# Optimization experiments

Hardware: AMD Instinct MI355X
Metric: run time of the kernel (lower is better)

## Reference

```python
import jax, jax.numpy as jnp
import numpy as np

N_MSB = 4
WB = 8       # weight bits
ABNM = 8     # activation bits for non-MVM ops
NL = 0.1     # noise level
B, IN, H = 256, 1024, 1024


def pact_a(x, a):
    # sign(x) * 0.5 * (|x| - ||x|-a| + a)  == sign(x)*min(|x|, a) for a>0
    return jnp.sign(x) * 0.5 * (jnp.abs(x) - jnp.abs(jnp.abs(x) - a) + a)


def _quant_val(x, bits, x_range):
    step = 2.0 ** (bits - 1)
    x01 = jnp.clip(x / x_range, -1.0 + 1.0 / step, 1.0 - 1.0 / step)
    return jnp.round(x01 * step) / step * x_range


def quant_ste(x, bits, x_range):
    # QuantFunc: straight-through estimator (identity grad wrt x, none wrt range)
    return x + jax.lax.stop_gradient(_quant_val(x, bits, x_range) - x)


def bitsplit(x, n_msb):
    # x in [0,1] -> n_msb binary planes stacked on axis 0, plus beta coefficients
    l1 = 2.0 ** n_msb - 1.0
    ys, betas = [], []
    for i in range(n_msb):
        l2 = 2.0 ** (n_msb - (i + 1))
        betas.append(l2 / l1)
        ys.append(jnp.mod(jnp.floor(jnp.round(l1 * x) / l2), 2.0))
    return jnp.stack(ys), jnp.asarray(betas, dtype=x.dtype)


def noisy_qmm(x, w, b, eps_w, eps_b):
    # CustomMM_bmm: quantized weights + gaussian noise in fwd; STE-style bwd.
    w_eff = w + jax.lax.stop_gradient(_quant_val(w, WB, 1.0) - w + eps_w * jnp.max(w) * NL)
    b_eff = b + jax.lax.stop_gradient(_quant_val(b, WB, 1.0) - b + eps_b * jnp.max(b) * NL)
    return jnp.einsum('nbi,nio->nbo', x, w_eff) + b_eff  # [n_msb, B, 4H]


def lstm_cell_q_bs(input, hx, cx, weight_ih, weight_hh, bias_ih, bias_hh,
                   eps_w_ih, eps_w_hh, eps_b_ih, eps_b_hh,
                   a1, a3, a4, a5, a6, a7, a8, a9, a10, a11):
    inp01 = (pact_a(input, a1) + a1) / (a1 * 2.0)            # [B, IN] in [0,1]
    inp_msb, beta = bitsplit(inp01, N_MSB)                   # [n_msb,B,IN], [n_msb]
    o1 = noisy_qmm(inp_msb, weight_ih, bias_ih, eps_w_ih, eps_b_ih)
    o2 = noisy_qmm(inp_msb, weight_hh, bias_hh, eps_w_hh, eps_b_hh)
    out = (o1 > 0.5).astype(inp01.dtype) + (o2 > 0.5).astype(inp01.dtype)
    gates = jnp.einsum('n,nbo->bo', beta, out)               # part1; part2 undefined in source -> 0
    i, j, f, o = jnp.split(gates, 4, axis=1)                 # each [B, H]
    forget_gate_out = quant_ste(pact_a(jax.nn.sigmoid(f), a3), ABNM, a3)
    input_gate_out = quant_ste(pact_a(jax.nn.sigmoid(i), a4), ABNM, a4)
    activation_out = quant_ste(pact_a(jnp.tanh(j), a5), ABNM, a5)
    output_gate_out = quant_ste(pact_a(jax.nn.sigmoid(o), a6), ABNM, a6)
    gated_cell = quant_ste(pact_a(cx * forget_gate_out, a7), ABNM, a7)
    activated_input = quant_ste(pact_a(input_gate_out * activation_out, a8), ABNM, a8)
    new_c = quant_ste(pact_a(gated_cell + activated_input, a9), ABNM, a9)
    activated_cell = quant_ste(pact_a(jnp.tanh(new_c), a10), ABNM, a10)
    new_h = quant_ste(pact_a(activated_cell * output_gate_out, a11), ABNM, a11)
    return new_h, new_c


def setup_inputs() -> dict:
    key = jax.random.key(0)
    ks = jax.random.split(key, 12)
    d = {
        'input': jax.random.normal(ks[0], (B, IN), jnp.float32),
        'hx': jax.random.normal(ks[1], (B, H), jnp.float32),
        'cx': jax.random.normal(ks[2], (B, H), jnp.float32),
        'weight_ih': jax.random.normal(ks[3], (N_MSB, IN, 4 * H), jnp.float32),
        'weight_hh': jax.random.normal(ks[4], (N_MSB, IN, 4 * H), jnp.float32),
        'bias_ih': jax.random.normal(ks[5], (N_MSB, 1, 4 * H), jnp.float32),
        'bias_hh': jax.random.normal(ks[6], (N_MSB, 1, 4 * H), jnp.float32),
        'eps_w_ih': jax.random.normal(ks[7], (N_MSB, IN, 4 * H), jnp.float32),
        'eps_w_hh': jax.random.normal(ks[8], (N_MSB, IN, 4 * H), jnp.float32),
        'eps_b_ih': jax.random.normal(ks[9], (N_MSB, 1, 4 * H), jnp.float32),
        'eps_b_hh': jax.random.normal(ks[10], (N_MSB, 1, 4 * H), jnp.float32),
    }
    a_init = {'a1': 128.0, 'a3': 1.0, 'a4': 1.0, 'a5': 1.0, 'a6': 1.0,
              'a7': 4.0, 'a8': 1.0, 'a9': 4.0, 'a10': 1.0, 'a11': 4.0}
    for name, v in a_init.items():
        d[name] = jnp.array([v], jnp.float32)
    return d


def reference(input, hx, cx, weight_ih, weight_hh, bias_ih, bias_hh,
              eps_w_ih, eps_w_hh, eps_b_ih, eps_b_hh,
              a1, a3, a4, a5, a6, a7, a8, a9, a10, a11):
    return lstm_cell_q_bs(input, hx, cx, weight_ih, weight_hh, bias_ih, bias_hh,
                          eps_w_ih, eps_w_hh, eps_b_ih, eps_b_hh,
                          a1, a3, a4, a5, a6, a7, a8, a9, a10, a11)
```

## Files before the change

### kernel.cpp

```cpp
#include <hip/hip_runtime.h>
#include <hip/hip_bf16.h>
#include <math.h>

typedef int   v4i __attribute__((ext_vector_type(4)));
typedef float v4f __attribute__((ext_vector_type(4)));

#define B_DIM   256
#define IN_DIM  1024
#define H4      4096
#define NPLANE  4
#define WELEM   (NPLANE * IN_DIM * H4)
#define XELEM   (B_DIM * IN_DIM)

#define WS_THRESH_OFF 64
#define WS_X_OFF      (64 + 262144)
#define WS_CMP_OFF    (64 + 262144 + 1048576)

#define SYNC_LDS() __asm__ volatile("s_waitcnt lgkmcnt(0)\n\ts_barrier" ::: "memory")

__global__ void k_max(const float* __restrict__ wih, const float* __restrict__ whh,
                      const float* __restrict__ bih, const float* __restrict__ bhh,
                      float* __restrict__ outm) {
  int b = blockIdx.x, t = threadIdx.x;
  const v4f* p; int slot; size_t base; int iters;
  if (b < 2048)      { p = (const v4f*)wih; slot = 0; base = (size_t)b * 2048;          iters = 8;  }
  else if (b < 4096) { p = (const v4f*)whh; slot = 1; base = (size_t)(b - 2048) * 2048; iters = 8;  }
  else if (b == 4096){ p = (const v4f*)bih; slot = 2; base = 0;                          iters = 16; }
  else               { p = (const v4f*)bhh; slot = 3; base = 0;                          iters = 16; }
  float m = -3.4e38f;
#pragma unroll 4
  for (int it = 0; it < iters; ++it) {
    v4f v = p[base + (size_t)it * 256 + t];
    m = fmaxf(m, fmaxf(fmaxf(v.x, v.y), fmaxf(v.z, v.w)));
  }
#pragma unroll
  for (int off = 32; off >= 1; off >>= 1) m = fmaxf(m, __shfl_down(m, off, 64));
  __shared__ float sm[4];
  int w = t >> 6, ln = t & 63;
  if (ln == 0) sm[w] = m;
  __syncthreads();
  if (t == 0) {
    m = fmaxf(fmaxf(sm[0], sm[1]), fmaxf(sm[2], sm[3]));
    atomicMax((int*)&outm[slot], __float_as_int(m));
  }
}

__global__ void k_prep(const float* __restrict__ input,
                       const float* __restrict__ bih, const float* __restrict__ bhh,
                       const float* __restrict__ ebih, const float* __restrict__ ebhh,
                       const float* __restrict__ a1p, const float* __restrict__ maxm,
                       double* __restrict__ thresh, signed char* __restrict__ X) {
  int gid = blockIdx.x * 256 + threadIdx.x;
  if (blockIdx.x < 1024) {
    float a1 = a1p[0];
    float x = input[gid];
    float t = fabsf(x), u = fabsf(t - a1);
    float sg = (x > 0.f) ? 0.5f : ((x < 0.f) ? -0.5f : 0.f);
    float p = sg * ((t - u) + a1);
    float inp01 = (p + a1) / (a1 * 2.0f);
    float q = rintf(15.0f * inp01);
    int qi = (int)q;
#pragma unroll
    for (int pl = 0; pl < 4; ++pl)
      X[pl * XELEM + gid] = (signed char)((qi >> (3 - pl)) & 1);
  } else {
    int i2 = gid - 262144;
    int s = i2 >> 14; int r = i2 & 16383;
    const float* bp = s ? bhh : bih;
    const float* ep = s ? ebhh : ebih;
    float mb = maxm[2 + s];
    float bv = bp[r], ev = ep[r];
    float xc = fminf(fmaxf(bv, -0.9921875f), 0.9921875f);
    float qv = rintf(xc * 128.f) * 0.0078125f;
    float noise = (ev * mb) * 0.1f;
    float beff = bv + ((qv - bv) + noise);
    thresh[i2] = 0.5 - (double)beff;
  }
}

__global__ __launch_bounds__(512, 4) void k_gemm(
    const float* __restrict__ Wih, const float* __restrict__ Whh,
    const float* __restrict__ Eih, const float* __restrict__ Ehh,
    const float* __restrict__ maxm, const double* __restrict__ thresh,
    const signed char* __restrict__ X, unsigned char* __restrict__ cmp) {
  const int ntile = blockIdx.x;
  const int sp = blockIdx.y;
  const int s = sp >> 2, plane = sp & 3;
  const float* W = s ? Whh : Wih;
  const float* E = s ? Ehh : Eih;
  const float maxw = maxm[s];

  const int tid = threadIdx.x;
  const int wave = tid >> 6, lane = tid & 63, quad = lane >> 4, l15 = lane & 15;

  __shared__ __align__(16) signed char Blds[2][4][32][80];

  v4i acc[4][2][2];
#pragma unroll
  for (int d = 0; d < 4; ++d)
#pragma unroll
    for (int m = 0; m < 2; ++m)
#pragma unroll
      for (int n = 0; n < 2; ++n) acc[d][m][n] = (v4i){0, 0, 0, 0};

  const int sn  = tid & 31;
  const int skq = tid >> 5;
  const float* Wt = W + (size_t)plane * (IN_DIM * H4) + (size_t)(skq * 4) * H4 + ntile * 32 + sn;
  const float* Et = E + (size_t)plane * (IN_DIM * H4) + (size_t)(skq * 4) * H4 + ntile * 32 + sn;

  const signed char* Xp = X + plane * XELEM;
  const int arow0 = wave * 32 + l15;

  auto cw = [&](const float wv[4], const float ev[4], int bf) {
    int pk[4] = {0, 0, 0, 0};
#pragma unroll
    for (int j = 0; j < 4; ++j) {
      float w = wv[j], evv = ev[j];
      float xc = fminf(fmaxf(w, -0.9921875f), 0.9921875f);
      float qv = rintf(xc * 128.f) * 0.0078125f;
      float noise = (evv * maxw) * 0.1f;
      float a = w + ((qv - w) + noise);
      float x0 = a * 8.f;    float f0 = rintf(x0); float r0 = x0 - f0;
      float x1 = r0 * 128.f; float f1 = rintf(x1); float r1 = x1 - f1;
      float x2 = r1 * 128.f; float f2 = rintf(x2); float r2 = x2 - f2;
      float x3 = r2 * 128.f; float f3 = rintf(x3);
      pk[0] |= ((int)f0 & 0xff) << (8 * j);
      pk[1] |= ((int)f1 & 0xff) << (8 * j);
      pk[2] |= ((int)f2 & 0xff) << (8 * j);
      pk[3] |= ((int)f3 & 0xff) << (8 * j);
    }
#pragma unroll
    for (int d = 0; d < 4; ++d)
      *(int*)&Blds[bf][d][sn][skq * 4] = pk[d];
  };

  auto loadWE = [&](int ck, float wv[4], float ev[4]) {
    size_t o = (size_t)(ck * 64) * H4;
#pragma unroll
    for (int j = 0; j < 4; ++j) { wv[j] = Wt[o + (size_t)j * H4]; ev[j] = Et[o + (size_t)j * H4]; }
  };

  float wA[4], eA[4], wB[4], eB[4];
  loadWE(0, wA, eA);
  loadWE(1, wB, eB);
  cw(wA, eA, 0);
  v4i afr[2], anx[2];
  afr[0] = *(const v4i*)(Xp + (arow0)      * IN_DIM + quad * 16);
  afr[1] = *(const v4i*)(Xp + (arow0 + 16) * IN_DIM + quad * 16);
  anx[0] = *(const v4i*)(Xp + (arow0)      * IN_DIM + 64 + quad * 16);
  anx[1] = *(const v4i*)(Xp + (arow0 + 16) * IN_DIM + 64 + quad * 16);
  SYNC_LDS();

#pragma unroll
  for (int ch = 0; ch < 16; ++ch) {
    const int buf = ch & 1;
    float wN[4], eN[4];
    v4i aN[2];
    if (ch < 14) {
      loadWE(ch + 2, wN, eN);
      aN[0] = *(const v4i*)(Xp + (arow0)      * IN_DIM + (ch + 2) * 64 + quad * 16);
      aN[1] = *(const v4i*)(Xp + (arow0 + 16) * IN_DIM + (ch + 2) * 64 + quad * 16);
    }
#pragma unroll
    for (int d = 0; d < 4; ++d) {
#pragma unroll
      for (int ns = 0; ns < 2; ++ns) {
        v4i bfr = *(const v4i*)&Blds[buf][d][ns * 16 + l15][quad * 16];
        acc[d][0][ns] = __builtin_amdgcn_mfma_i32_16x16x64_i8(afr[0], bfr, acc[d][0][ns], 0, 0, 0);
        acc[d][1][ns] = __builtin_amdgcn_mfma_i32_16x16x64_i8(afr[1], bfr, acc[d][1][ns], 0, 0, 0);
      }
    }
    if (ch < 15) cw(wB, eB, buf ^ 1);
#pragma unroll
    for (int j = 0; j < 4; ++j) { wB[j] = wN[j]; eB[j] = eN[j]; }
    afr[0] = anx[0]; afr[1] = anx[1];
    anx[0] = aN[0];  anx[1] = aN[1];
    SYNC_LDS();
  }

  const double inv = 1.0 / 16777216.0;
  const double* thp = thresh + (size_t)sp * H4;
  unsigned char* cp = cmp + (size_t)sp * B_DIM * H4;
#pragma unroll
  for (int ms = 0; ms < 2; ++ms) {
#pragma unroll
    for (int ns = 0; ns < 2; ++ns) {
      int col = ntile * 32 + ns * 16 + l15;
      double th = thp[col];
#pragma unroll
      for (int r = 0; r < 4; ++r) {
        long long T = ((long long)acc[0][ms][ns][r] << 21) + ((long long)acc[1][ms][ns][r] << 14)
                    + ((long long)acc[2][ms][ns][r] << 7)  +  (long long)acc[3][ms][ns][r];
        int row = wave * 32 + ms * 16 + quad * 4 + r;
        cp[(size_t)row * H4 + col] = ((double)T * inv > th) ? 1 : 0;
      }
    }
  }
}

__device__ __forceinline__ float pact_(float x, float a) {
  float t = fabsf(x), u = fabsf(t - a);
  float sg = (x > 0.f) ? 0.5f : ((x < 0.f) ? -0.5f : 0.f);
  return sg * ((t - u) + a);
}
__device__ __forceinline__ float quant_(float x, float a) {
  float xr = x / a;
  xr = fminf(fmaxf(xr, -0.9921875f), 0.9921875f);
  return rintf(xr * 128.f) * 0.0078125f * a;
}
__device__ __forceinline__ float sigm_(float x) { return 1.0f / (1.0f + expf(-x)); }

__global__ void k_pointwise(const unsigned char* __restrict__ cmp, const float* __restrict__ cx,
                            const float* a3, const float* a4, const float* a5, const float* a6,
                            const float* a7, const float* a8, const float* a9, const float* a10,
                            const float* a11, float* __restrict__ out) {
  int idx = blockIdx.x * 256 + threadIdx.x;
  int b = idx >> 10, h = idx & 1023;
  float g[4];
#pragma unroll
  for (int gi = 0; gi < 4; ++gi) {
    int col = gi * 1024 + h;
    float acc = 0.f;
#pragma unroll
    for (int n = 0; n < 4; ++n) {
      int o = (int)cmp[((size_t)(0 * 4 + n) * B_DIM + b) * H4 + col]
            + (int)cmp[((size_t)(1 * 4 + n) * B_DIM + b) * H4 + col];
      float beta = (float)(8 >> n) / 15.0f;
      acc = acc + beta * (float)o;
    }
    g[gi] = acc;
  }
  float fg = quant_(pact_(sigm_(g[2]), a3[0]), a3[0]);
  float ig = quant_(pact_(sigm_(g[0]), a4[0]), a4[0]);
  float ac = quant_(pact_(tanhf(g[1]), a5[0]), a5[0]);
  float og = quant_(pact_(sigm_(g[3]), a6[0]), a6[0]);
  float cxv = cx[idx];
  float gc = quant_(pact_(cxv * fg, a7[0]), a7[0]);
  float ai = quant_(pact_(ig * ac, a8[0]), a8[0]);
  float nc = quant_(pact_(gc + ai, a9[0]), a9[0]);
  float acl = quant_(pact_(tanhf(nc), a10[0]), a10[0]);
  float nh = quant_(pact_(acl * og, a11[0]), a11[0]);
  out[idx] = nh;
  out[XELEM + idx] = nc;
}

extern "C" void kernel_launch(void* const* d_in, const int* in_sizes, int n_in,
                              void* d_out, int out_size, void* d_ws, size_t ws_size,
                              hipStream_t stream) {
  (void)in_sizes; (void)n_in; (void)out_size; (void)ws_size;
  const float* input = (const float*)d_in[0];
  const float* cx    = (const float*)d_in[2];
  const float* wih   = (const float*)d_in[3];
  const float* whh   = (const float*)d_in[4];
  const float* bih   = (const float*)d_in[5];
  const float* bhh   = (const float*)d_in[6];
  const float* ewih  = (const float*)d_in[7];
  const float* ewhh  = (const float*)d_in[8];
  const float* ebih  = (const float*)d_in[9];
  const float* ebhh  = (const float*)d_in[10];
  const float* a1    = (const float*)d_in[11];
  const float* a3    = (const float*)d_in[12];
  const float* a4    = (const float*)d_in[13];
  const float* a5    = (const float*)d_in[14];
  const float* a6    = (const float*)d_in[15];
  const float* a7    = (const float*)d_in[16];
  const float* a8    = (const float*)d_in[17];
  const float* a9    = (const float*)d_in[18];
  const float* a10   = (const float*)d_in[19];
  const float* a11   = (const float*)d_in[20];
  float* out = (float*)d_out;

  char* ws = (char*)d_ws;
  float*         maxm   = (float*)ws;
  double*        thresh = (double*)(ws + WS_THRESH_OFF);
  signed char*   X      = (signed char*)(ws + WS_X_OFF);
  unsigned char* cmp    = (unsigned char*)(ws + WS_CMP_OFF);

  hipMemsetAsync(ws, 0, 64, stream);
  k_max<<<4098, 256, 0, stream>>>(wih, whh, bih, bhh, maxm);
  k_prep<<<1152, 256, 0, stream>>>(input, bih, bhh, ebih, ebhh, a1, maxm, thresh, X);
  k_gemm<<<dim3(128, 8), 512, 0, stream>>>(wih, whh, ewih, ewhh, maxm, thresh, X, cmp);
  k_pointwise<<<1024, 256, 0, stream>>>(cmp, cx, a3, a4, a5, a6, a7, a8, a9, a10, a11, out);
}
```

Measured before the change: 346.3 us.

## Stream W/E tiles into LDS via async global_load_lds triple buffer; two-pass max

The GEMM kernel now loads weight and noise tiles straight into a three-deep LDS ring with global_load_lds. Waits are explicit vmcnt counts, and each chunk is digitized from LDS into a double-buffered int8 tile before the MFMAs run. This removes register staging and is meant to overlap HBM streaming of the fp32 weights with compute. The max reduction changes from 4098 blocks with atomicMax plus a memset to 1026 blocks writing partial maxima, followed by a single-block reduce kernel. This adds LDS pressure (48KB raw) and an extra kernel launch, and the hand-written vmcnt counts must be exactly right.

Measured after the change: 347.0 us. Within noise of the previous version (+0.2%).

```diff
diff --git a/kernel.cpp b/kernel.cpp
--- a/kernel.cpp
+++ b/kernel.cpp
@@ -8,25 +8,25 @@
 #define B_DIM   256
 #define IN_DIM  1024
 #define H4      4096
-#define NPLANE  4
-#define WELEM   (NPLANE * IN_DIM * H4)
 #define XELEM   (B_DIM * IN_DIM)
 
 #define WS_THRESH_OFF 64
 #define WS_X_OFF      (64 + 262144)
 #define WS_CMP_OFF    (64 + 262144 + 1048576)
 
-#define SYNC_LDS() __asm__ volatile("s_waitcnt lgkmcnt(0)\n\ts_barrier" ::: "memory")
+#define BAR()   __asm__ volatile("s_barrier" ::: "memory")
+#define BARL()  __asm__ volatile("s_waitcnt lgkmcnt(0)\n\ts_barrier" ::: "memory")
+#define WVM(n)  __asm__ volatile("s_waitcnt vmcnt(" #n ")" ::: "memory")
 
 __global__ void k_max(const float* __restrict__ wih, const float* __restrict__ whh,
                       const float* __restrict__ bih, const float* __restrict__ bhh,
-                      float* __restrict__ outm) {
+                      float* __restrict__ part) {
   int b = blockIdx.x, t = threadIdx.x;
-  const v4f* p; int slot; size_t base; int iters;
-  if (b < 2048)      { p = (const v4f*)wih; slot = 0; base = (size_t)b * 2048;          iters = 8;  }
-  else if (b < 4096) { p = (const v4f*)whh; slot = 1; base = (size_t)(b - 2048) * 2048; iters = 8;  }
-  else if (b == 4096){ p = (const v4f*)bih; slot = 2; base = 0;                          iters = 16; }
-  else               { p = (const v4f*)bhh; slot = 3; base = 0;                          iters = 16; }
+  const v4f* p; size_t base; int iters;
+  if (b < 512)       { p = (const v4f*)wih; base = (size_t)b * 8192;         iters = 32; }
+  else if (b < 1024) { p = (const v4f*)whh; base = (size_t)(b - 512) * 8192; iters = 32; }
+  else if (b == 1024){ p = (const v4f*)bih; base = 0;                         iters = 16; }
+  else               { p = (const v4f*)bhh; base = 0;                         iters = 16; }
   float m = -3.4e38f;
 #pragma unroll 4
   for (int it = 0; it < iters; ++it) {
@@ -39,10 +39,24 @@
   int w = t >> 6, ln = t & 63;
   if (ln == 0) sm[w] = m;
   __syncthreads();
-  if (t == 0) {
-    m = fmaxf(fmaxf(sm[0], sm[1]), fmaxf(sm[2], sm[3]));
-    atomicMax((int*)&outm[slot], __float_as_int(m));
-  }
+  if (t == 0) part[b] = fmaxf(fmaxf(sm[0], sm[1]), fmaxf(sm[2], sm[3]));
+}
+
+__global__ void k_max2(const float* __restrict__ part, float* __restrict__ maxm) {
+  int t = threadIdx.x;
+  __shared__ float sm[4];
+#pragma unroll
+  for (int slot = 0; slot < 2; ++slot) {
+    float m = fmaxf(part[slot * 512 + t], part[slot * 512 + 256 + t]);
+#pragma unroll
+    for (int off = 32; off >= 1; off >>= 1) m = fmaxf(m, __shfl_down(m, off, 64));
+    int w = t >> 6, ln = t & 63;
+    if (ln == 0) sm[w] = m;
+    __syncthreads();
+    if (t == 0) maxm[slot] = fmaxf(fmaxf(sm[0], sm[1]), fmaxf(sm[2], sm[3]));
+    __syncthreads();
+  }
+  if (t == 0) { maxm[2] = part[1024]; maxm[3] = part[1025]; }
 }
 
 __global__ void k_prep(const float* __restrict__ input,
@@ -93,7 +107,8 @@
   const int tid = threadIdx.x;
   const int wave = tid >> 6, lane = tid & 63, quad = lane >> 4, l15 = lane & 15;
 
-  __shared__ __align__(16) signed char Blds[2][4][32][80];
+  __shared__ __align__(16) float raw[3][4096];
+  __shared__ __align__(16) signed char dbuf[2][4][32][80];
 
   v4i acc[4][2][2];
 #pragma unroll
@@ -103,22 +118,36 @@
 #pragma unroll
       for (int n = 0; n < 2; ++n) acc[d][m][n] = (v4i){0, 0, 0, 0};
 
-  const int sn  = tid & 31;
-  const int skq = tid >> 5;
-  const float* Wt = W + (size_t)plane * (IN_DIM * H4) + (size_t)(skq * 4) * H4 + ntile * 32 + sn;
-  const float* Et = E + (size_t)plane * (IN_DIM * H4) + (size_t)(skq * 4) * H4 + ntile * 32 + sn;
+  const int dr = wave * 8 + (lane >> 3);
+  const int dc = (lane & 7) * 4;
+  const size_t tbase = (size_t)plane * (IN_DIM * H4) + (size_t)ntile * 32;
+  const float* gW = W + tbase + (size_t)dr * H4 + dc;
+  const float* gE = E + tbase + (size_t)dr * H4 + dc;
 
   const signed char* Xp = X + plane * XELEM;
   const int arow0 = wave * 32 + l15;
 
-  auto cw = [&](const float wv[4], const float ev[4], int bf) {
+  auto dma = [&](int ch) {
+    const int rb = ch % 3;
+    const float* gw = gW + (size_t)(ch * 64) * H4;
+    const float* ge = gE + (size_t)(ch * 64) * H4;
+    __builtin_amdgcn_global_load_lds((const unsigned int*)gw,
+                                     (unsigned int*)&raw[rb][wave * 256], 16, 0, 0);
+    __builtin_amdgcn_global_load_lds((const unsigned int*)ge,
+                                     (unsigned int*)&raw[rb][2048 + wave * 256], 16, 0, 0);
+  };
+
+  const int sn = tid & 31, skq = tid >> 5;
+  auto digitize = [&](int ch) {
+    const int rb = ch % 3, db = ch & 1;
     int pk[4] = {0, 0, 0, 0};
 #pragma unroll
     for (int j = 0; j < 4; ++j) {
-      float w = wv[j], evv = ev[j];
+      float w  = raw[rb][(skq * 4 + j) * 32 + sn];
+      float ev = raw[rb][2048 + (skq * 4 + j) * 32 + sn];
       float xc = fminf(fmaxf(w, -0.9921875f), 0.9921875f);
       float qv = rintf(xc * 128.f) * 0.0078125f;
-      float noise = (evv * maxw) * 0.1f;
+      float noise = (ev * maxw) * 0.1f;
       float a = w + ((qv - w) + noise);
       float x0 = a * 8.f;    float f0 = rintf(x0); float r0 = x0 - f0;
       float x1 = r0 * 128.f; float f1 = rintf(x1); float r1 = x1 - f1;
@@ -131,51 +160,43 @@
     }
 #pragma unroll
     for (int d = 0; d < 4; ++d)
-      *(int*)&Blds[bf][d][sn][skq * 4] = pk[d];
+      *(int*)&dbuf[db][d][sn][skq * 4] = pk[d];
   };
 
-  auto loadWE = [&](int ck, float wv[4], float ev[4]) {
-    size_t o = (size_t)(ck * 64) * H4;
-#pragma unroll
-    for (int j = 0; j < 4; ++j) { wv[j] = Wt[o + (size_t)j * H4]; ev[j] = Et[o + (size_t)j * H4]; }
+  auto loadA = [&](int ch, v4i a[2]) {
+    a[0] = *(const v4i*)(Xp + (size_t)(arow0)      * IN_DIM + ch * 64 + quad * 16);
+    a[1] = *(const v4i*)(Xp + (size_t)(arow0 + 16) * IN_DIM + ch * 64 + quad * 16);
   };
 
-  float wA[4], eA[4], wB[4], eB[4];
-  loadWE(0, wA, eA);
-  loadWE(1, wB, eB);
-  cw(wA, eA, 0);
-  v4i afr[2], anx[2];
-  afr[0] = *(const v4i*)(Xp + (arow0)      * IN_DIM + quad * 16);
-  afr[1] = *(const v4i*)(Xp + (arow0 + 16) * IN_DIM + quad * 16);
-  anx[0] = *(const v4i*)(Xp + (arow0)      * IN_DIM + 64 + quad * 16);
-  anx[1] = *(const v4i*)(Xp + (arow0 + 16) * IN_DIM + 64 + quad * 16);
-  SYNC_LDS();
+  auto mma = [&](int ch, const v4i a[2]) {
+    const int db = ch & 1;
+#pragma unroll
+    for (int d = 0; d < 4; ++d)
+#pragma unroll
+      for (int ns = 0; ns < 2; ++ns) {
+        v4i bfr = *(const v4i*)&dbuf[db][d][ns * 16 + l15][quad * 16];
+        acc[d][0][ns] = __builtin_amdgcn_mfma_i32_16x16x64_i8(a[0], bfr, acc[d][0][ns], 0, 0, 0);
+        acc[d][1][ns] = __builtin_amdgcn_mfma_i32_16x16x64_i8(a[1], bfr, acc[d][1][ns], 0, 0, 0);
+      }
+  };
+
+  v4i aCur[2], aNxt[2];
+  dma(0);
+  loadA(0, aCur);
+  dma(1);
 
 #pragma unroll
   for (int ch = 0; ch < 16; ++ch) {
-    const int buf = ch & 1;
-    float wN[4], eN[4];
-    v4i aN[2];
-    if (ch < 14) {
-      loadWE(ch + 2, wN, eN);
-      aN[0] = *(const v4i*)(Xp + (arow0)      * IN_DIM + (ch + 2) * 64 + quad * 16);
-      aN[1] = *(const v4i*)(Xp + (arow0 + 16) * IN_DIM + (ch + 2) * 64 + quad * 16);
-    }
-#pragma unroll
-    for (int d = 0; d < 4; ++d) {
-#pragma unroll
-      for (int ns = 0; ns < 2; ++ns) {
-        v4i bfr = *(const v4i*)&Blds[buf][d][ns * 16 + l15][quad * 16];
-        acc[d][0][ns] = __builtin_amdgcn_mfma_i32_16x16x64_i8(afr[0], bfr, acc[d][0][ns], 0, 0, 0);
-        acc[d][1][ns] = __builtin_amdgcn_mfma_i32_16x16x64_i8(afr[1], bfr, acc[d][1][ns], 0, 0, 0);
-      }
-    }
-    if (ch < 15) cw(wB, eB, buf ^ 1);
-#pragma unroll
-    for (int j = 0; j < 4; ++j) { wB[j] = wN[j]; eB[j] = eN[j]; }
-    afr[0] = anx[0]; afr[1] = anx[1];
-    anx[0] = aN[0];  anx[1] = aN[1];
-    SYNC_LDS();
+    if (ch < 15) loadA(ch + 1, aNxt);
+    if (ch < 14) dma(ch + 2);
+    if (ch < 14)       WVM(8);
+    else if (ch == 14) WVM(6);
+    else               WVM(2);
+    BAR();
+    digitize(ch);
+    BARL();
+    mma(ch, aCur);
+    aCur[0] = aNxt[0]; aCur[1] = aNxt[1];
   }
 
   const double inv = 1.0 / 16777216.0;
@@ -275,9 +296,10 @@
   double*        thresh = (double*)(ws + WS_THRESH_OFF);
   signed char*   X      = (signed char*)(ws + WS_X_OFF);
   unsigned char* cmp    = (unsigned char*)(ws + WS_CMP_OFF);
-
-  hipMemsetAsync(ws, 0, 64, stream);
-  k_max<<<4098, 256, 0, stream>>>(wih, whh, bih, bhh, maxm);
+  float*         part   = (float*)(ws + WS_CMP_OFF);
+
+  k_max<<<1026, 256, 0, stream>>>(wih, whh, bih, bhh, part);
+  k_max2<<<1, 256, 0, stream>>>(part, maxm);
   k_prep<<<1152, 256, 0, stream>>>(input, bih, bhh, ebih, ebhh, a1, maxm, thresh, X);
   k_gemm<<<dim3(128, 8), 512, 0, stream>>>(wih, whh, ewih, ewhh, maxm, thresh, X, cmp);
   k_pointwise<<<1024, 256, 0, stream>>>(cmp, cx, a3, a4, a5, a6, a7, a8, a9, a10, a11, out);
```
